# Kernel optimization log

Hardware: AMD Instinct MI355X
Metric: run time of the kernel (lower is better)

Reference implementation:

```python
import jax, jax.numpy as jnp
import numpy as np

N_NODES = 100000
N_EDGES = 1600000
HIDDEN = 64
IN_CH = 6  # 3 (direction) + 3 (node feature part)
BN_EPS = 1e-5


def setup_inputs() -> dict:
    key = jax.random.key(0)
    ks = jax.random.split(key, 16)
    inp = {
        "x": jax.random.normal(ks[0], (N_NODES, 3), dtype=jnp.float32),
        "pos": jax.random.normal(ks[1], (N_NODES, 3), dtype=jnp.float32),
        "edge_index": jax.random.randint(ks[2], (2, N_EDGES), 0, N_NODES, dtype=jnp.int64),
    }
    dims = [IN_CH, HIDDEN, HIDDEN, HIDDEN]
    for i in range(3):
        din, dout = dims[i], dims[i + 1]
        inp[f"W{i+1}"] = jax.random.normal(ks[3 + 4 * i], (din, dout), dtype=jnp.float32) * (1.0 / np.sqrt(din))
        inp[f"b{i+1}"] = jnp.zeros((dout,), dtype=jnp.float32)
        inp[f"g{i+1}"] = jnp.ones((dout,), dtype=jnp.float32)   # BN gamma
        inp[f"be{i+1}"] = jnp.zeros((dout,), dtype=jnp.float32)  # BN beta
    return inp


def _mlp_layer(h, W, b, g, be):
    # Linear -> ReLU -> BatchNorm1d (training mode, biased variance like torch)
    h = jax.nn.relu(h @ W + b)
    mu = jnp.mean(h, axis=0)
    var = jnp.mean((h - mu) ** 2, axis=0)
    return g * (h - mu) * jax.lax.rsqrt(var + BN_EPS) + be


def reference(x, pos, edge_index, W1, b1, g1, be1, W2, b2, g2, be2, W3, b3, g3, be3):
    n = x.shape[0]
    xp = jnp.concatenate([pos, x], axis=1)             # [N, 3+F]
    src, dst = edge_index[0], edge_index[1]            # j = src, i = dst (PyG source_to_target)
    x_j = xp[src]                                      # [E, 3+F]
    x_i = xp[dst]
    direction = x_j[:, :3] - x_i[:, :3]                # [E, 3]
    # NOTE: source uses torch.norm with no dim => single global scalar norm
    direction = direction / jnp.linalg.norm(direction)
    h = jnp.concatenate([direction, x_i[:, 3:]], axis=-1)  # [E, IN_CH]
    h = _mlp_layer(h, W1, b1, g1, be1)
    h = _mlp_layer(h, W2, b2, g2, be2)
    h = _mlp_layer(h, W3, b3, g3, be3)                 # [E, HIDDEN]
    out = jax.ops.segment_max(h, dst, num_segments=n)  # scatter-max aggregation
    out = jnp.where(jnp.isfinite(out), out, 0.0)       # PyG fills empty segments with 0
    return out
```

## Files before the change

### kernel.cpp

```cpp
#include <hip/hip_runtime.h>
#include <stdint.h>

typedef unsigned short u16;
typedef unsigned int u32;
typedef __attribute__((ext_vector_type(8))) short short8;
typedef __attribute__((ext_vector_type(4))) float floatx4;

#define BN_EPS 1e-5f
#define NPB 64
#define NPB_SHIFT 6
#define NBMAX 2048

__device__ __forceinline__ float bf2f(u16 u) { return __uint_as_float(((unsigned)u) << 16); }
__device__ __forceinline__ u16 f2bf(float f) {
  unsigned u = __float_as_uint(f);
  u += 0x7FFFu + ((u >> 16) & 1u);
  return (u16)(u >> 16);
}

__global__ void k_init(float* __restrict__ stats, u32* __restrict__ bucketTotal) {
  for (int i = threadIdx.x; i < 1024; i += blockDim.x) stats[i] = 0.f;
  for (int i = threadIdx.x; i < NBMAX + 1; i += blockDim.x) bucketTotal[i] = 0u;
}

__global__ void k_norm_hist(const int* __restrict__ ei, const float* __restrict__ pos,
                            int E, int NB, float* __restrict__ stats,
                            u32* __restrict__ bucketTotal) {
  __shared__ u32 lh[NBMAX];
  __shared__ float red[16];
  for (int i = threadIdx.x; i < NB; i += blockDim.x) lh[i] = 0u;
  __syncthreads();
  int tid = blockIdx.x * blockDim.x + threadIdx.x;
  int stride = gridDim.x * blockDim.x;
  float acc = 0.f;
  for (int e = tid; e < E; e += stride) {
    int s = ei[e], d = ei[E + e];
    float d0 = pos[3 * s + 0] - pos[3 * d + 0];
    float d1 = pos[3 * s + 1] - pos[3 * d + 1];
    float d2 = pos[3 * s + 2] - pos[3 * d + 2];
    acc = fmaf(d0, d0, acc);
    acc = fmaf(d1, d1, acc);
    acc = fmaf(d2, d2, acc);
    atomicAdd(&lh[d >> NPB_SHIFT], 1u);
  }
#pragma unroll
  for (int off = 32; off > 0; off >>= 1) acc += __shfl_down(acc, off, 64);
  if ((threadIdx.x & 63) == 0) red[threadIdx.x >> 6] = acc;
  __syncthreads();
  if (threadIdx.x == 0) {
    float s = 0.f;
    for (int w = 0; w < (int)(blockDim.x >> 6); w++) s += red[w];
    atomicAdd(&stats[0], s);
  }
  for (int i = threadIdx.x; i < NB; i += blockDim.x)
    if (lh[i]) atomicAdd(&bucketTotal[i], lh[i]);
}

__global__ void k_scan(const u32* __restrict__ bucketTotal, u32* __restrict__ base,
                       u32* __restrict__ cursor, int NB) {
  int lane = threadIdx.x;
  u32 run = 0;
  for (int b0 = 0; b0 < NB; b0 += 64) {
    int b = b0 + lane;
    u32 v = (b < NB) ? bucketTotal[b] : 0u;
    u32 s = v;
#pragma unroll
    for (int off = 1; off < 64; off <<= 1) {
      u32 t = __shfl_up(s, off, 64);
      if (lane >= off) s += t;
    }
    u32 excl = run + s - v;
    if (b < NB) { base[b] = excl; cursor[b] = excl; }
    run += __shfl(s, 63, 64);
  }
  if (lane == 0) base[NB] = run;
}

__global__ void k_place(const int* __restrict__ ei, int E, int NB,
                        u32* __restrict__ cursor, uint2* __restrict__ sorted2) {
  __shared__ u32 lh[NBMAX];
  __shared__ u32 lbase[NBMAX];
  for (int i = threadIdx.x; i < NB; i += blockDim.x) lh[i] = 0u;
  __syncthreads();
  int tid = blockIdx.x * blockDim.x + threadIdx.x;
  int stride = gridDim.x * blockDim.x;
  for (int e = tid; e < E; e += stride) atomicAdd(&lh[ei[E + e] >> NPB_SHIFT], 1u);
  __syncthreads();
  for (int i = threadIdx.x; i < NB; i += blockDim.x) {
    u32 c = lh[i];
    lbase[i] = c ? atomicAdd(&cursor[i], c) : 0u;
    lh[i] = 0u;
  }
  __syncthreads();
  for (int e = tid; e < E; e += stride) {
    int s = ei[e];
    int d = ei[E + e];
    int b = d >> NPB_SHIFT;
    u32 slot = lbase[b] + atomicAdd(&lh[b], 1u);
    sorted2[slot] = make_uint2((u32)s, (u32)d);
  }
}

__global__ __launch_bounds__(256) void k_layer1(
    const int* __restrict__ ei, const float* __restrict__ pos,
    const float* __restrict__ x, const float* __restrict__ W1,
    const float* __restrict__ b1, u16* __restrict__ h,
    const float* __restrict__ stats, float* __restrict__ gsum,
    float* __restrict__ gsq, int E, const uint2* __restrict__ sorted2) {
  __shared__ float in6[6][256];
  __shared__ float ssum[64], ssq[64];
  float invn = 1.0f / sqrtf(stats[0]);
  int t = threadIdx.x;
  int lane = t & 63;
  int wv = t >> 6;
  float w[6];
#pragma unroll
  for (int k = 0; k < 6; k++) w[k] = W1[k * 64 + lane];
  float bias = b1[lane];
  float psum = 0.f, psq = 0.f;

  int chunks = (E + 255) >> 8;
  for (int c = blockIdx.x; c < chunks; c += gridDim.x) {
    long e0 = (long)c << 8;
    int e = (int)e0 + t;
    float v[6] = {0.f, 0.f, 0.f, 0.f, 0.f, 0.f};
    if (e < E) {
      int s, d;
      if (sorted2) {
        uint2 sd = sorted2[e];
        s = (int)sd.x;
        d = (int)sd.y;
      } else {
        s = ei[e];
        d = ei[E + e];
      }
      float p0 = pos[3 * s + 0], p1 = pos[3 * s + 1], p2 = pos[3 * s + 2];
      float q0 = pos[3 * d + 0], q1 = pos[3 * d + 1], q2 = pos[3 * d + 2];
      v[0] = (p0 - q0) * invn;
      v[1] = (p1 - q1) * invn;
      v[2] = (p2 - q2) * invn;
      v[3] = x[3 * d + 0];
      v[4] = x[3 * d + 1];
      v[5] = x[3 * d + 2];
    }
    __syncthreads();
#pragma unroll
    for (int k = 0; k < 6; k++) in6[k][t] = v[k];
    __syncthreads();
    int lim = E - (int)e0;
    if (lim > 256) lim = 256;
    int base = wv * 64;
#pragma unroll 4
    for (int i = 0; i < 64; i++) {
      int el = base + i;
      if (el >= lim) break;
      float acc = bias;
#pragma unroll
      for (int k = 0; k < 6; k++) acc = fmaf(in6[k][el], w[k], acc);
      acc = fmaxf(acc, 0.f);
      u16 hb = f2bf(acc);
      h[(e0 + el) * 64 + lane] = hb;
      float hf = bf2f(hb);
      psum += hf;
      psq = fmaf(hf, hf, psq);
    }
  }
  if (t < 64) { ssum[t] = 0.f; ssq[t] = 0.f; }
  __syncthreads();
  atomicAdd(&ssum[lane], psum);
  atomicAdd(&ssq[lane], psq);
  __syncthreads();
  if (t < 64) {
    atomicAdd(&gsum[t], ssum[t]);
    atomicAdd(&gsq[t], ssq[t]);
  }
}

__global__ __launch_bounds__(256) void k_layer_mfma(
    u16* h, const float* __restrict__ W, const float* __restrict__ b,
    const float* __restrict__ gsum_in, const float* __restrict__ gsq_in,
    const float* __restrict__ g_in, const float* __restrict__ be_in, float invE,
    float* __restrict__ gsum, float* __restrict__ gsq, int E) {
  __shared__ float sc_s[64], sh_s[64];
  if (threadIdx.x < 64) {
    int c = threadIdx.x;
    float mu = gsum_in[c] * invE;
    float var = gsq_in[c] * invE - mu * mu;
    float s = g_in[c] * rsqrtf(var + BN_EPS);
    sc_s[c] = s;
    sh_s[c] = be_in[c] - mu * s;
  }
  __syncthreads();

  int lane = threadIdx.x & 63;
  int m = lane & 15;
  int q = lane >> 4;

  short8 bf[4][2];
  float bias[4];
#pragma unroll
  for (int t = 0; t < 4; t++) {
    int n = t * 16 + m;
    float bb = b[n];
    for (int k = 0; k < 64; k++) bb = fmaf(sh_s[k], W[k * 64 + n], bb);
    bias[t] = bb;
#pragma unroll
    for (int s = 0; s < 2; s++)
#pragma unroll
      for (int j = 0; j < 8; j++) {
        int k = s * 32 + q * 8 + j;
        bf[t][s][j] = (short)f2bf(W[k * 64 + n] * sc_s[k]);
      }
  }

  float psum[4] = {0.f, 0.f, 0.f, 0.f}, psq[4] = {0.f, 0.f, 0.f, 0.f};

  int tiles = E >> 4;
  int gw = ((int)blockIdx.x * (blockDim.x >> 6)) + (threadIdx.x >> 6);
  int nw = (int)gridDim.x * (blockDim.x >> 6);

  for (int tile = gw; tile < tiles; tile += nw) {
    long e0 = (long)tile * 16;
    const u16* rowp = h + (e0 + m) * 64 + q * 8;
    short8 a0 = *(const short8*)(rowp);
    short8 a1 = *(const short8*)(rowp + 32);
    floatx4 acc[4];
#pragma unroll
    for (int t = 0; t < 4; t++) acc[t] = (floatx4){0.f, 0.f, 0.f, 0.f};
#pragma unroll
    for (int t = 0; t < 4; t++)
      acc[t] = __builtin_amdgcn_mfma_f32_16x16x32_bf16(a0, bf[t][0], acc[t], 0, 0, 0);
#pragma unroll
    for (int t = 0; t < 4; t++)
      acc[t] = __builtin_amdgcn_mfma_f32_16x16x32_bf16(a1, bf[t][1], acc[t], 0, 0, 0);

#pragma unroll
    for (int t = 0; t < 4; t++) {
#pragma unroll
      for (int r = 0; r < 4; r++) {
        float v = acc[t][r] + bias[t];
        v = fmaxf(v, 0.f);
        u16 hb = f2bf(v);
        h[(e0 + q * 4 + r) * 64 + t * 16 + m] = hb;
        float hf = bf2f(hb);
        psum[t] += hf;
        psq[t] = fmaf(hf, hf, psq[t]);
      }
    }
  }

#pragma unroll
  for (int t = 0; t < 4; t++) {
    psum[t] += __shfl_xor(psum[t], 16, 64);
    psum[t] += __shfl_xor(psum[t], 32, 64);
    psq[t] += __shfl_xor(psq[t], 16, 64);
    psq[t] += __shfl_xor(psq[t], 32, 64);
  }
  __shared__ float ssum[64], ssq[64];
  if (threadIdx.x < 64) { ssum[threadIdx.x] = 0.f; ssq[threadIdx.x] = 0.f; }
  __syncthreads();
  if (q == 0) {
#pragma unroll
    for (int t = 0; t < 4; t++) {
      atomicAdd(&ssum[t * 16 + m], psum[t]);
      atomicAdd(&ssq[t * 16 + m], psq[t]);
    }
  }
  __syncthreads();
  if (threadIdx.x < 64) {
    atomicAdd(&gsum[threadIdx.x], ssum[threadIdx.x]);
    atomicAdd(&gsq[threadIdx.x], ssq[threadIdx.x]);
  }
}

__global__ __launch_bounds__(256) void k_layer3_max(
    const u16* __restrict__ h, const uint2* __restrict__ sorted2,
    const u32* __restrict__ base, const float* __restrict__ W,
    const float* __restrict__ b, const float* __restrict__ gsum_in,
    const float* __restrict__ gsq_in, const float* __restrict__ g_in,
    const float* __restrict__ be_in, float invE, float* __restrict__ gsum,
    float* __restrict__ gsq, const float* __restrict__ g3,
    u32* __restrict__ outk, int N) {
  __shared__ float sc_s[64], sh_s[64];
  __shared__ u32 tile[64 * 65];
  __shared__ float ssum[64], ssq[64];
  if (threadIdx.x < 64) {
    int c = threadIdx.x;
    float mu = gsum_in[c] * invE;
    float var = gsq_in[c] * invE - mu * mu;
    float s = g_in[c] * rsqrtf(var + BN_EPS);
    sc_s[c] = s;
    sh_s[c] = be_in[c] - mu * s;
    ssum[c] = 0.f;
    ssq[c] = 0.f;
  }
  for (int i = threadIdx.x; i < 64 * 65; i += blockDim.x) tile[i] = 0u;
  __syncthreads();

  int lane = threadIdx.x & 63;
  int m = lane & 15;
  int q = lane >> 4;
  int wv = threadIdx.x >> 6;

  short8 bf[4][2];
  float bias[4];
  u32 xmask[4];
#pragma unroll
  for (int t = 0; t < 4; t++) {
    int n = t * 16 + m;
    float bb = b[n];
    for (int k = 0; k < 64; k++) bb = fmaf(sh_s[k], W[k * 64 + n], bb);
    bias[t] = bb;
    xmask[t] = (g3[n] < 0.f) ? 0xFFFFu : 0u;
#pragma unroll
    for (int s = 0; s < 2; s++)
#pragma unroll
      for (int j = 0; j < 8; j++) {
        int k = s * 32 + q * 8 + j;
        bf[t][s][j] = (short)f2bf(W[k * 64 + n] * sc_s[k]);
      }
  }

  int bb_ = blockIdx.x;
  int start = (int)base[bb_];
  int end = (int)base[bb_ + 1];
  float psum[4] = {0.f, 0.f, 0.f, 0.f}, psq[4] = {0.f, 0.f, 0.f, 0.f};

  for (int i0 = start + wv * 16; i0 < end; i0 += 64) {
    int rr = i0 + m;
    if (rr > end - 1) rr = end - 1;
    const u16* rowp = h + (long)rr * 64 + q * 8;
    short8 a0 = *(const short8*)(rowp);
    short8 a1 = *(const short8*)(rowp + 32);
    floatx4 acc[4];
#pragma unroll
    for (int t = 0; t < 4; t++) acc[t] = (floatx4){0.f, 0.f, 0.f, 0.f};
#pragma unroll
    for (int t = 0; t < 4; t++)
      acc[t] = __builtin_amdgcn_mfma_f32_16x16x32_bf16(a0, bf[t][0], acc[t], 0, 0, 0);
#pragma unroll
    for (int t = 0; t < 4; t++)
      acc[t] = __builtin_amdgcn_mfma_f32_16x16x32_bf16(a1, bf[t][1], acc[t], 0, 0, 0);

    u32 lnr[4];
#pragma unroll
    for (int r = 0; r < 4; r++) {
      int sl = i0 + q * 4 + r;
      lnr[r] = (sl < end) ? (sorted2[sl].y & (u32)(NPB - 1)) : 0xFFFFFFFFu;
    }
#pragma unroll
    for (int t = 0; t < 4; t++) {
      int c = t * 16 + m;
      u32 curln = 0xFFFFFFFFu, curkey = 0u;
#pragma unroll
      for (int r = 0; r < 4; r++) {
        if (lnr[r] == 0xFFFFFFFFu) continue;
        float v = acc[t][r] + bias[t];
        v = fmaxf(v, 0.f);
        u16 hb = f2bf(v);
        float hf = bf2f(hb);
        psum[t] += hf;
        psq[t] = fmaf(hf, hf, psq[t]);
        u32 key = ((u32)hb ^ xmask[t]) | 0x10000u;
        if (lnr[r] == curln) {
          curkey = key > curkey ? key : curkey;
        } else {
          if (curln != 0xFFFFFFFFu) atomicMax(&tile[curln * 65 + c], curkey);
          curln = lnr[r];
          curkey = key;
        }
      }
      if (curln != 0xFFFFFFFFu) atomicMax(&tile[curln * 65 + c], curkey);
    }
  }

#pragma unroll
  for (int t = 0; t < 4; t++) {
    psum[t] += __shfl_xor(psum[t], 16, 64);
    psum[t] += __shfl_xor(psum[t], 32, 64);
    psq[t] += __shfl_xor(psq[t], 16, 64);
    psq[t] += __shfl_xor(psq[t], 32, 64);
  }
  __syncthreads();
  if (q == 0) {
#pragma unroll
    for (int t = 0; t < 4; t++) {
      atomicAdd(&ssum[t * 16 + m], psum[t]);
      atomicAdd(&ssq[t * 16 + m], psq[t]);
    }
  }
  __syncthreads();
  if (threadIdx.x < 64) {
    if (ssum[threadIdx.x] != 0.f) atomicAdd(&gsum[threadIdx.x], ssum[threadIdx.x]);
    if (ssq[threadIdx.x] != 0.f) atomicAdd(&gsq[threadIdx.x], ssq[threadIdx.x]);
  }
  int node0 = bb_ * NPB;
  for (int l = threadIdx.x; l < NPB * 64; l += blockDim.x) {
    int node = node0 + (l >> 6);
    if (node < N) outk[(long)node * 64 + (l & 63)] = tile[(l >> 6) * 65 + (l & 63)];
  }
}

__global__ void k_final(u32* __restrict__ outk, const float* __restrict__ gsum3,
                        const float* __restrict__ gsq3, const float* __restrict__ g3,
                        const float* __restrict__ be3, float invE, long n) {
  int c = threadIdx.x & 63;
  float mu = gsum3[c] * invE;
  float var = gsq3[c] * invE - mu * mu;
  float sc = g3[c] * rsqrtf(var + BN_EPS);
  float sh = be3[c] - mu * sc;
  u32 me = (g3[c] < 0.f) ? 0xFFFFu : 0u;
  long i = (long)blockIdx.x * blockDim.x + threadIdx.x;
  long stride = (long)gridDim.x * blockDim.x;
  for (long j = i; j < n; j += stride) {
    u32 k = outk[j];
    float v = (k == 0u) ? 0.f : fmaf(bf2f((u16)((k & 0xFFFFu) ^ me)), sc, sh);
    ((float*)outk)[j] = v;
  }
}

__global__ void k_initout(float* __restrict__ outf, long n, float* __restrict__ stats,
                          u32* __restrict__ bucketTotal) {
  long i = (long)blockIdx.x * blockDim.x + threadIdx.x;
  long stride = (long)gridDim.x * blockDim.x;
  for (long j = i; j < n; j += stride) outf[j] = __uint_as_float(0xFF800000u);
  if (i < 1024) stats[i] = 0.f;
  if (i < NBMAX + 1) bucketTotal[i] = 0u;
}
__global__ void k_scatter(const int* __restrict__ ei, const u16* __restrict__ h,
                          const float* __restrict__ gsum3, const float* __restrict__ gsq3,
                          const float* __restrict__ g3, const float* __restrict__ be3,
                          float invE, float* outf, int E) {
  int lane = threadIdx.x & 63;
  int gw = ((int)blockIdx.x * (blockDim.x >> 6)) + (threadIdx.x >> 6);
  int nw = (int)gridDim.x * (blockDim.x >> 6);
  float mu = gsum3[lane] * invE;
  float var = gsq3[lane] * invE - mu * mu;
  float sc = g3[lane] * rsqrtf(var + BN_EPS);
  float sh = be3[lane] - mu * sc;
  for (int e = gw; e < E; e += nw) {
    int d = ei[E + e];
    float v = fmaf(bf2f(h[(long)e * 64 + lane]), sc, sh);
    float* addr = outf + (long)d * 64 + lane;
    if (v >= 0.f)
      atomicMax((int*)addr, __float_as_int(v));
    else
      atomicMin((unsigned int*)addr, __float_as_uint(v));
  }
}
__global__ void k_out(float* __restrict__ outf, long n) {
  long i = (long)blockIdx.x * blockDim.x + threadIdx.x;
  long stride = (long)gridDim.x * blockDim.x;
  for (long j = i; j < n; j += stride) {
    float v = outf[j];
    unsigned u = __float_as_uint(v);
    if ((u & 0x7F800000u) == 0x7F800000u) v = 0.f;
    outf[j] = v;
  }
}

extern "C" void kernel_launch(void* const* d_in, const int* in_sizes, int n_in,
                              void* d_out, int out_size, void* d_ws, size_t ws_size,
                              hipStream_t stream) {
  const float* x = (const float*)d_in[0];
  const float* pos = (const float*)d_in[1];
  const int* ei = (const int*)d_in[2];
  const float* W1 = (const float*)d_in[3];
  const float* b1 = (const float*)d_in[4];
  const float* g1 = (const float*)d_in[5];
  const float* be1 = (const float*)d_in[6];
  const float* W2 = (const float*)d_in[7];
  const float* b2 = (const float*)d_in[8];
  const float* g2 = (const float*)d_in[9];
  const float* be2 = (const float*)d_in[10];
  const float* W3 = (const float*)d_in[11];
  const float* b3 = (const float*)d_in[12];
  const float* g3 = (const float*)d_in[13];
  const float* be3 = (const float*)d_in[14];

  int N = in_sizes[0] / 3;
  int E = in_sizes[2] / 2;
  int NB = (N + NPB - 1) / NPB;
  long n_out = (long)N * 64;

  char* wsb = (char*)d_ws;
  u16* h = (u16*)wsb;
  size_t off = (size_t)E * 64 * 2;
  float* stats = (float*)(wsb + off);
  off += 1024 * 4;
  u32* bucketTotal = (u32*)(wsb + off);
  off += (NBMAX + 1) * 4;
  u32* baseArr = (u32*)(wsb + off);
  off += (NBMAX + 1) * 4;
  u32* cursor = (u32*)(wsb + off);
  off += NBMAX * 4;
  off = (off + 7) & ~(size_t)7;
  uint2* sorted2 = (uint2*)(wsb + off);
  off += (size_t)E * 8;
  size_t need = off;

  float* gsum1 = stats + 64, * gsq1 = stats + 128;
  float* gsum2 = stats + 192, * gsq2 = stats + 256;
  float* gsum3 = stats + 320, * gsq3 = stats + 384;

  float* outf = (float*)d_out;
  float invE = 1.0f / (float)E;
  bool binned = (ws_size >= need) && (NB <= NBMAX);

  if (binned) {
    k_init<<<1, 1024, 0, stream>>>(stats, bucketTotal);
    k_norm_hist<<<256, 256, 0, stream>>>(ei, pos, E, NB, stats, bucketTotal);
    k_scan<<<1, 64, 0, stream>>>(bucketTotal, baseArr, cursor, NB);
    k_place<<<256, 256, 0, stream>>>(ei, E, NB, cursor, sorted2);
    k_layer1<<<1024, 256, 0, stream>>>(ei, pos, x, W1, b1, h, stats, gsum1, gsq1, E, sorted2);
    k_layer_mfma<<<1024, 256, 0, stream>>>(h, W2, b2, gsum1, gsq1, g1, be1, invE, gsum2, gsq2, E);
    k_layer3_max<<<NB, 256, 0, stream>>>(h, sorted2, baseArr, W3, b3, gsum2, gsq2, g2, be2,
                                         invE, gsum3, gsq3, g3, (u32*)outf, N);
    k_final<<<1024, 256, 0, stream>>>((u32*)outf, gsum3, gsq3, g3, be3, invE, n_out);
  } else {
    k_initout<<<4096, 256, 0, stream>>>(outf, n_out, stats, bucketTotal);
    k_norm_hist<<<256, 256, 0, stream>>>(ei, pos, E, NB <= NBMAX ? NB : 1, stats, bucketTotal);
    k_layer1<<<1024, 256, 0, stream>>>(ei, pos, x, W1, b1, h, stats, gsum1, gsq1, E, (const uint2*)nullptr);
    k_layer_mfma<<<1024, 256, 0, stream>>>(h, W2, b2, gsum1, gsq1, g1, be1, invE, gsum2, gsq2, E);
    k_layer_mfma<<<1024, 256, 0, stream>>>(h, W3, b3, gsum2, gsq2, g2, be2, invE, gsum3, gsq3, E);
    k_scatter<<<2048, 256, 0, stream>>>(ei, h, gsum3, gsq3, g3, be3, invE, outf, E);
    k_out<<<2048, 256, 0, stream>>>(outf, n_out);
  }
}
```

Baseline: 499.4 us.

## Replace per-bucket LDS max tiles with grid-stride global atomicMax in layer 3

Layer 3 switches from one block per 64-node bucket (accumulating max keys in a shared-memory tile, then writing it out) to a fixed 1024-block grid-stride loop over edge tiles that applies atomicMax directly to the global output. The output buffer is now zeroed in an enlarged k_init launch. The aim is to fix load imbalance from uneven bucket sizes and drop the LDS tile init and copy-out, at the cost of many global atomics with possible contention across blocks.

```diff
diff --git a/kernel.cpp b/kernel.cpp
--- a/kernel.cpp
+++ b/kernel.cpp
@@ -18,9 +18,13 @@
   return (u16)(u >> 16);
 }
 
-__global__ void k_init(float* __restrict__ stats, u32* __restrict__ bucketTotal) {
-  for (int i = threadIdx.x; i < 1024; i += blockDim.x) stats[i] = 0.f;
-  for (int i = threadIdx.x; i < NBMAX + 1; i += blockDim.x) bucketTotal[i] = 0u;
+__global__ void k_init(float* __restrict__ stats, u32* __restrict__ bucketTotal,
+                       u32* __restrict__ outk, long n) {
+  long i = (long)blockIdx.x * blockDim.x + threadIdx.x;
+  long stride = (long)gridDim.x * blockDim.x;
+  for (long j = i; j < n; j += stride) outk[j] = 0u;
+  if (i < 1024) stats[i] = 0.f;
+  if (i <= NBMAX) bucketTotal[i] = 0u;
 }
 
 __global__ void k_norm_hist(const int* __restrict__ ei, const float* __restrict__ pos,
@@ -275,15 +279,12 @@
 
 __global__ __launch_bounds__(256) void k_layer3_max(
     const u16* __restrict__ h, const uint2* __restrict__ sorted2,
-    const u32* __restrict__ base, const float* __restrict__ W,
-    const float* __restrict__ b, const float* __restrict__ gsum_in,
-    const float* __restrict__ gsq_in, const float* __restrict__ g_in,
-    const float* __restrict__ be_in, float invE, float* __restrict__ gsum,
-    float* __restrict__ gsq, const float* __restrict__ g3,
-    u32* __restrict__ outk, int N) {
+    const float* __restrict__ W, const float* __restrict__ b,
+    const float* __restrict__ gsum_in, const float* __restrict__ gsq_in,
+    const float* __restrict__ g_in, const float* __restrict__ be_in, float invE,
+    float* __restrict__ gsum, float* __restrict__ gsq,
+    const float* __restrict__ g3, u32* __restrict__ outk, int E) {
   __shared__ float sc_s[64], sh_s[64];
-  __shared__ u32 tile[64 * 65];
-  __shared__ float ssum[64], ssq[64];
   if (threadIdx.x < 64) {
     int c = threadIdx.x;
     float mu = gsum_in[c] * invE;
@@ -291,16 +292,12 @@
     float s = g_in[c] * rsqrtf(var + BN_EPS);
     sc_s[c] = s;
     sh_s[c] = be_in[c] - mu * s;
-    ssum[c] = 0.f;
-    ssq[c] = 0.f;
-  }
-  for (int i = threadIdx.x; i < 64 * 65; i += blockDim.x) tile[i] = 0u;
+  }
   __syncthreads();
 
   int lane = threadIdx.x & 63;
   int m = lane & 15;
   int q = lane >> 4;
-  int wv = threadIdx.x >> 6;
 
   short8 bf[4][2];
   float bias[4];
@@ -321,15 +318,17 @@
       }
   }
 
-  int bb_ = blockIdx.x;
-  int start = (int)base[bb_];
-  int end = (int)base[bb_ + 1];
   float psum[4] = {0.f, 0.f, 0.f, 0.f}, psq[4] = {0.f, 0.f, 0.f, 0.f};
 
-  for (int i0 = start + wv * 16; i0 < end; i0 += 64) {
-    int rr = i0 + m;
-    if (rr > end - 1) rr = end - 1;
-    const u16* rowp = h + (long)rr * 64 + q * 8;
+  int tiles = (E + 15) >> 4;
+  int gw = ((int)blockIdx.x * (blockDim.x >> 6)) + (threadIdx.x >> 6);
+  int nw = (int)gridDim.x * (blockDim.x >> 6);
+
+  for (int tile = gw; tile < tiles; tile += nw) {
+    long e0 = (long)tile * 16;
+    long er = e0 + m;
+    if (er >= E) er = E - 1;
+    const u16* rowp = h + er * 64 + q * 8;
     short8 a0 = *(const short8*)(rowp);
     short8 a1 = *(const short8*)(rowp + 32);
     floatx4 acc[4];
@@ -342,19 +341,19 @@
     for (int t = 0; t < 4; t++)
       acc[t] = __builtin_amdgcn_mfma_f32_16x16x32_bf16(a1, bf[t][1], acc[t], 0, 0, 0);
 
-    u32 lnr[4];
+    u32 nd[4];
 #pragma unroll
     for (int r = 0; r < 4; r++) {
-      int sl = i0 + q * 4 + r;
-      lnr[r] = (sl < end) ? (sorted2[sl].y & (u32)(NPB - 1)) : 0xFFFFFFFFu;
+      long sl = e0 + q * 4 + r;
+      nd[r] = (sl < E) ? sorted2[sl].y : 0xFFFFFFFFu;
     }
 #pragma unroll
     for (int t = 0; t < 4; t++) {
       int c = t * 16 + m;
-      u32 curln = 0xFFFFFFFFu, curkey = 0u;
+      u32 curnd = 0xFFFFFFFFu, curkey = 0u;
 #pragma unroll
       for (int r = 0; r < 4; r++) {
-        if (lnr[r] == 0xFFFFFFFFu) continue;
+        if (nd[r] == 0xFFFFFFFFu) continue;
         float v = acc[t][r] + bias[t];
         v = fmaxf(v, 0.f);
         u16 hb = f2bf(v);
@@ -362,15 +361,15 @@
         psum[t] += hf;
         psq[t] = fmaf(hf, hf, psq[t]);
         u32 key = ((u32)hb ^ xmask[t]) | 0x10000u;
-        if (lnr[r] == curln) {
+        if (nd[r] == curnd) {
           curkey = key > curkey ? key : curkey;
         } else {
-          if (curln != 0xFFFFFFFFu) atomicMax(&tile[curln * 65 + c], curkey);
-          curln = lnr[r];
+          if (curnd != 0xFFFFFFFFu) atomicMax(&outk[(long)curnd * 64 + c], curkey);
+          curnd = nd[r];
           curkey = key;
         }
       }
-      if (curln != 0xFFFFFFFFu) atomicMax(&tile[curln * 65 + c], curkey);
+      if (curnd != 0xFFFFFFFFu) atomicMax(&outk[(long)curnd * 64 + c], curkey);
     }
   }
 
@@ -381,6 +380,8 @@
     psq[t] += __shfl_xor(psq[t], 16, 64);
     psq[t] += __shfl_xor(psq[t], 32, 64);
   }
+  __shared__ float ssum[64], ssq[64];
+  if (threadIdx.x < 64) { ssum[threadIdx.x] = 0.f; ssq[threadIdx.x] = 0.f; }
   __syncthreads();
   if (q == 0) {
 #pragma unroll
@@ -391,13 +392,8 @@
   }
   __syncthreads();
   if (threadIdx.x < 64) {
-    if (ssum[threadIdx.x] != 0.f) atomicAdd(&gsum[threadIdx.x], ssum[threadIdx.x]);
-    if (ssq[threadIdx.x] != 0.f) atomicAdd(&gsq[threadIdx.x], ssq[threadIdx.x]);
-  }
-  int node0 = bb_ * NPB;
-  for (int l = threadIdx.x; l < NPB * 64; l += blockDim.x) {
-    int node = node0 + (l >> 6);
-    if (node < N) outk[(long)node * 64 + (l & 63)] = tile[(l >> 6) * 65 + (l & 63)];
+    atomicAdd(&gsum[threadIdx.x], ssum[threadIdx.x]);
+    atomicAdd(&gsq[threadIdx.x], ssq[threadIdx.x]);
   }
 }
 
@@ -508,14 +504,14 @@
   bool binned = (ws_size >= need) && (NB <= NBMAX);
 
   if (binned) {
-    k_init<<<1, 1024, 0, stream>>>(stats, bucketTotal);
+    k_init<<<2048, 256, 0, stream>>>(stats, bucketTotal, (u32*)outf, n_out);
     k_norm_hist<<<256, 256, 0, stream>>>(ei, pos, E, NB, stats, bucketTotal);
     k_scan<<<1, 64, 0, stream>>>(bucketTotal, baseArr, cursor, NB);
     k_place<<<256, 256, 0, stream>>>(ei, E, NB, cursor, sorted2);
     k_layer1<<<1024, 256, 0, stream>>>(ei, pos, x, W1, b1, h, stats, gsum1, gsq1, E, sorted2);
     k_layer_mfma<<<1024, 256, 0, stream>>>(h, W2, b2, gsum1, gsq1, g1, be1, invE, gsum2, gsq2, E);
-    k_layer3_max<<<NB, 256, 0, stream>>>(h, sorted2, baseArr, W3, b3, gsum2, gsq2, g2, be2,
-                                         invE, gsum3, gsq3, g3, (u32*)outf, N);
+    k_layer3_max<<<1024, 256, 0, stream>>>(h, sorted2, W3, b3, gsum2, gsq2, g2, be2,
+                                           invE, gsum3, gsq3, g3, (u32*)outf, E);
     k_final<<<1024, 256, 0, stream>>>((u32*)outf, gsum3, gsq3, g3, be3, invE, n_out);
   } else {
     k_initout<<<4096, 256, 0, stream>>>(outf, n_out, stats, bucketTotal);
```

Measured after the change: 652.6 us. 1.31x slower.
